# Optimization experiments

Hardware: AMD Instinct MI355X
Metric: run time of the kernel (lower is better)

The kernel has to match this reference:

```python
import jax, jax.numpy as jnp
import numpy as np

N_NODES = 50000
N_EDGES = 800000
N_GRAPHS = 512
IN_DIM, HID, OUT_DIM = 128, 96, 10
N_CONV = 4


def setup_inputs() -> dict:
    key = jax.random.key(0)
    ks = jax.random.split(key, 16)
    s = 0.05
    inp = {
        "x": jax.random.normal(ks[0], (N_NODES, IN_DIM), dtype=jnp.float32),
        "edge_index": jax.random.randint(ks[1], (2, N_EDGES), 0, N_NODES, dtype=jnp.int64),
        "batch": jnp.sort(jax.random.randint(ks[2], (N_NODES,), 0, N_GRAPHS, dtype=jnp.int64)),
        # encoder MLP (2 layers: in->hid, hid->hid)
        "enc_W0": jax.random.normal(ks[3], (IN_DIM, HID), dtype=jnp.float32) * s,
        "enc_b0": jnp.zeros((HID,), dtype=jnp.float32),
        "enc_W1": jax.random.normal(ks[4], (HID, HID), dtype=jnp.float32) * s,
        "enc_b1": jnp.zeros((HID,), dtype=jnp.float32),
        # stacked GCNConv weights
        "conv_W": jax.random.normal(ks[5], (N_CONV, HID, HID), dtype=jnp.float32) * s,
        "conv_b": jnp.zeros((N_CONV, HID), dtype=jnp.float32),
        # decoder MLP (2 layers: hid->hid, hid->out)
        "dec_W0": jax.random.normal(ks[6], (HID, HID), dtype=jnp.float32) * s,
        "dec_b0": jnp.zeros((HID,), dtype=jnp.float32),
        "dec_W1": jax.random.normal(ks[7], (HID, OUT_DIM), dtype=jnp.float32) * s,
        "dec_b1": jnp.zeros((OUT_DIM,), dtype=jnp.float32),
    }
    return inp


def reference(x, edge_index, batch, enc_W0, enc_b0, enc_W1, enc_b1,
              conv_W, conv_b, dec_W0, dec_b0, dec_W1, dec_b1):
    n = x.shape[0]
    src, dst = edge_index[0], edge_index[1]  # source_to_target flow

    # encoder MLP (dropout is identity in eval mode)
    h = jax.nn.relu(x @ enc_W0 + enc_b0)
    h = h @ enc_W1 + enc_b1

    # GCN symmetric normalization with self-loops: deg[i] = in_degree + 1
    deg = jax.ops.segment_sum(jnp.ones_like(dst, dtype=h.dtype), dst, num_segments=n) + 1.0
    dinv = jax.lax.rsqrt(deg)                    # [N]
    edge_norm = (dinv[src] * dinv[dst])[:, None]  # [E,1]
    self_norm = (dinv * dinv)[:, None]            # [N,1] self-loop coefficient

    for l in range(conv_W.shape[0]):
        hw = h @ conv_W[l]                              # linear transform [N,HID]
        msg = hw[src] * edge_norm                       # gather + scale [E,HID]
        h = (jax.ops.segment_sum(msg, dst, num_segments=n)
             + hw * self_norm + conv_b[l])              # scatter-add + self-loop + bias
        h = jax.nn.relu(h)

    # global add pool over graphs in the batch
    g = jax.ops.segment_sum(h, batch, num_segments=N_GRAPHS)  # [G,HID]

    # decoder MLP
    g = jax.nn.relu(g @ dec_W0 + dec_b0)
    return g @ dec_W1 + dec_b1
```

## Files before the change

### kernel.cpp

```cpp
#include <hip/hip_runtime.h>

#define HID 96
#define INDIM 128
#define OUTDIM 10

typedef __attribute__((ext_vector_type(8))) short bf16x8;
typedef __attribute__((ext_vector_type(4))) float f32x4;

__device__ __forceinline__ unsigned short f2bf(float f) {
  unsigned int u = __float_as_uint(f);
  unsigned int r = (u + 0x7FFFu + ((u >> 16) & 1u)) >> 16;
  return (unsigned short)r;
}
__device__ __forceinline__ bf16x8 as_bf16x8(uint4 u) {
  union { uint4 a; bf16x8 b; } c; c.a = u; return c.b;
}
__device__ __forceinline__ float bflo(unsigned int u) { return __uint_as_float(u << 16); }
__device__ __forceinline__ float bfhi(unsigned int u) { return __uint_as_float(u & 0xFFFF0000u); }

__global__ __launch_bounds__(256) void k_prep(const float* __restrict__ x,
                                              unsigned int* __restrict__ xb, long long xu,
                                              int* __restrict__ cnt, int n, int XB,
                                              const float* __restrict__ encW0,
                                              const float* __restrict__ encW1,
                                              const float* __restrict__ convW,
                                              uint4* __restrict__ wp) {
  int b = blockIdx.x;
  if (b < XB) {
    long long i = (long long)b * 256 + threadIdx.x;
    if (i < xu) {
      float2 v = ((const float2*)x)[i];
      xb[i] = (unsigned int)f2bf(v.x) | ((unsigned int)f2bf(v.y) << 16);
    }
    if (i < n) cnt[i] = 0;
    return;
  }
  int bid = b - XB;
  int lane = threadIdx.x;
  if (lane >= 64) return;
  const float* Wsrc;
  int frag;
  if (bid < 24) { Wsrc = encW0; frag = bid; }
  else if (bid < 42) { Wsrc = encW1; frag = bid - 24; }
  else { int c = bid - 42; Wsrc = convW + (size_t)(c / 18) * HID * HID; frag = c % 18; }
  int ks = frag / 6, cf = frag % 6;
  int col = cf * 16 + (lane & 15);
  int k0 = ks * 32 + (lane >> 4) * 8;
  unsigned int u[4];
#pragma unroll
  for (int p = 0; p < 4; ++p) {
    float lo = Wsrc[(size_t)(k0 + 2 * p) * 96 + col];
    float hi = Wsrc[(size_t)(k0 + 2 * p + 1) * 96 + col];
    u[p] = (unsigned int)f2bf(lo) | ((unsigned int)f2bf(hi) << 16);
  }
  uint4 r; r.x = u[0]; r.y = u[1]; r.z = u[2]; r.w = u[3];
  wp[(size_t)bid * 64 + lane] = r;
}

__device__ __forceinline__ void scanA_body(int blk, const int* __restrict__ cnt, int n,
                                           int* __restrict__ bsum, float* __restrict__ dinv) {
  __shared__ int red[256];
  int t = threadIdx.x;
  int base = blk * 512;
  int v = 0;
  int i0 = base + t, i1 = base + 256 + t;
  if (i0 < n) { int c = cnt[i0]; v += c; dinv[i0] = rsqrtf((float)c + 1.0f); }
  if (i1 < n) { int c = cnt[i1]; v += c; dinv[i1] = rsqrtf((float)c + 1.0f); }
  red[t] = v;
  __syncthreads();
  for (int off = 128; off > 0; off >>= 1) {
    if (t < off) red[t] += red[t + off];
    __syncthreads();
  }
  if (t == 0) bsum[blk] = red[0];
}

template <int KS, bool RELU, bool BIAS, bool SCALE>
__device__ __forceinline__ void gemm_body(int blk, const uint4* __restrict__ Ab,
                                          const uint4* __restrict__ Bp,
                                          const float* __restrict__ bias,
                                          const float* __restrict__ rowscale,
                                          unsigned int* __restrict__ outB, int M) {
  int t = threadIdx.x, wid = t >> 6, lane = t & 63;
  int rowbase = blk * 64 + wid * 16;
  int arow = rowbase + (lane & 15);
  if (arow >= M) arow = M - 1;
  constexpr int RU4 = KS * 4;

  f32x4 acc[6];
#pragma unroll
  for (int cf = 0; cf < 6; ++cf)
#pragma unroll
    for (int j = 0; j < 4; ++j) acc[cf][j] = 0.f;

#pragma unroll
  for (int ks = 0; ks < KS; ++ks) {
    uint4 a = Ab[(size_t)arow * RU4 + ks * 4 + (lane >> 4)];
    bf16x8 af = as_bf16x8(a);
#pragma unroll
    for (int cf = 0; cf < 6; ++cf) {
      uint4 b = Bp[(size_t)(ks * 6 + cf) * 64 + lane];
      acc[cf] = __builtin_amdgcn_mfma_f32_16x16x32_bf16(af, as_bf16x8(b), acc[cf], 0, 0, 0);
    }
  }

  int rows[4]; float rs[4];
#pragma unroll
  for (int i = 0; i < 4; ++i) {
    rows[i] = rowbase + (lane >> 4) * 4 + i;
    int cr = rows[i] < M ? rows[i] : M - 1;
    rs[i] = SCALE ? rowscale[cr] : 1.f;
  }
#pragma unroll
  for (int cf = 0; cf < 6; ++cf) {
    int col = cf * 16 + (lane & 15);
    float bv = BIAS ? bias[col] : 0.f;
#pragma unroll
    for (int i = 0; i < 4; ++i) {
      float v = acc[cf][i] + bv;
      if (RELU) v = fmaxf(v, 0.f);
      v *= rs[i];
      float p = __shfl_xor(v, 1);
      if (!(lane & 1) && rows[i] < M) {
        unsigned int u = (unsigned int)f2bf(v) | ((unsigned int)f2bf(p) << 16);
        outB[(size_t)rows[i] * 48 + cf * 8 + ((lane & 15) >> 1)] = u;
      }
    }
  }
}

__global__ __launch_bounds__(256) void k_count_enc1(
    const int4* __restrict__ dst4, int E4, int* __restrict__ cnt, int* __restrict__ rank,
    int CB, const uint4* __restrict__ Ab, const uint4* __restrict__ Bp,
    const float* __restrict__ bias, unsigned int* __restrict__ outB, int M) {
  int b = blockIdx.x;
  if (b < CB) {
    int i = b * 256 + threadIdx.x;
    if (i >= E4) return;
    int4 d = dst4[i];
    int r0 = atomicAdd(&cnt[d.x], 1);
    int r1 = atomicAdd(&cnt[d.y], 1);
    int r2 = atomicAdd(&cnt[d.z], 1);
    int r3 = atomicAdd(&cnt[d.w], 1);
    ((int4*)rank)[i] = make_int4(r0, r1, r2, r3);
  } else {
    gemm_body<4, true, true, false>(b - CB, Ab, Bp, bias, nullptr, outB, M);
  }
}

__global__ __launch_bounds__(256) void k_scanA_enc2(
    const int* __restrict__ cnt, int n, int* __restrict__ bsum, float* __restrict__ dinv,
    int SB, const uint4* __restrict__ Ab, const uint4* __restrict__ Bp,
    const float* __restrict__ bias, unsigned int* __restrict__ outB, int M) {
  int b = blockIdx.x;
  if (b < SB) scanA_body(b, cnt, n, bsum, dinv);
  else gemm_body<3, false, true, false>(b - SB, Ab, Bp, bias, nullptr, outB, M);
}

__global__ __launch_bounds__(256) void k_scanC(const int* __restrict__ cnt, int n,
                                               const int* __restrict__ bsum, int nb,
                                               int* __restrict__ rowp, int Etot) {
  __shared__ int s[256];
  int b = blockIdx.x, t = threadIdx.x;
  int v0 = (t < b && t < nb) ? bsum[t] : 0;
  s[t] = v0;
  __syncthreads();
  for (int off = 128; off > 0; off >>= 1) {
    if (t < off) s[t] += s[t + off];
    __syncthreads();
  }
  int boff = s[0];
  __syncthreads();

  int base = b * 512;
  int i0 = base + 2 * t, i1 = i0 + 1;
  int c0 = (i0 < n) ? cnt[i0] : 0;
  int c1 = (i1 < n) ? cnt[i1] : 0;
  int pair = c0 + c1;
  s[t] = pair;
  __syncthreads();
  for (int off = 1; off < 256; off <<= 1) {
    int u = (t >= off) ? s[t - off] : 0;
    __syncthreads();
    s[t] += u;
    __syncthreads();
  }
  int excl = s[t] - pair + boff;
  if (i0 < n) rowp[i0] = excl;
  if (i1 < n) rowp[i1] = excl + c0;
  if (b == 0 && t == 0) rowp[n] = Etot;
}

__global__ __launch_bounds__(256) void k_fill_conv(
    const int4* __restrict__ src4, const int4* __restrict__ dst4,
    const int4* __restrict__ rank4, int E4, const int* __restrict__ rowp,
    int* __restrict__ csr, int FB, const uint4* __restrict__ Ab,
    const uint4* __restrict__ Bp, const float* __restrict__ rowscale,
    unsigned int* __restrict__ outB, int M) {
  int b = blockIdx.x;
  if (b < FB) {
    int i = b * 256 + threadIdx.x;
    if (i >= E4) return;
    int4 s = src4[i];
    int4 d = dst4[i];
    int4 r = rank4[i];
    csr[rowp[d.x] + r.x] = s.x;
    csr[rowp[d.y] + r.y] = s.y;
    csr[rowp[d.z] + r.z] = s.z;
    csr[rowp[d.w] + r.w] = s.w;
  } else {
    gemm_body<3, false, false, true>(b - FB, Ab, Bp, nullptr, rowscale, outB, M);
  }
}

template <int KS, bool RELU, bool BIAS, bool SCALE>
__global__ __launch_bounds__(256) void mfma_gemm(const uint4* __restrict__ Ab,
                                                 const uint4* __restrict__ Bp,
                                                 const float* __restrict__ bias,
                                                 const float* __restrict__ rowscale,
                                                 unsigned int* __restrict__ outB, int M) {
  gemm_body<KS, RELU, BIAS, SCALE>(blockIdx.x, Ab, Bp, bias, rowscale, outB, M);
}

__global__ __launch_bounds__(256) void k_agg(const unsigned int* __restrict__ hw_s,
                                             const int* __restrict__ rowp,
                                             const int* __restrict__ csr,
                                             const float* __restrict__ dinv,
                                             const float* __restrict__ bias,
                                             unsigned int* __restrict__ outB, int n) {
  int wave = threadIdx.x >> 6;
  int lane = threadIdx.x & 63;
  int node = blockIdx.x * 4 + wave;
  if (node >= n) return;
  int beg = rowp[node], end = rowp[node + 1];
  float acc0 = 0.f, acc1 = 0.f;
  bool act = lane < 48;
  int li = act ? lane : 0;
  int e = beg;
  for (; e + 16 <= end; e += 16) {
    unsigned int uu[16];
#pragma unroll
    for (int j = 0; j < 16; ++j) uu[j] = hw_s[(size_t)csr[e + j] * 48 + li];
    float a0 = 0.f, a1 = 0.f;
#pragma unroll
    for (int j = 0; j < 16; ++j) { a0 += bflo(uu[j]); a1 += bfhi(uu[j]); }
    acc0 += a0; acc1 += a1;
  }
  if (e < end) {
    unsigned int uu[16]; float m[16];
#pragma unroll
    for (int j = 0; j < 16; ++j) {
      int idx = e + j;
      bool ok = idx < end;
      int ci = csr[ok ? idx : end - 1];
      uu[j] = hw_s[(size_t)ci * 48 + li];
      m[j] = ok ? 1.f : 0.f;
    }
    float a0 = 0.f, a1 = 0.f;
#pragma unroll
    for (int j = 0; j < 16; ++j) { a0 += m[j] * bflo(uu[j]); a1 += m[j] * bfhi(uu[j]); }
    acc0 += a0; acc1 += a1;
  }
  if (act) {
    float di = dinv[node];
    unsigned int us = hw_s[(size_t)node * 48 + li];
    float2 bv = ((const float2*)bias)[li];
    float r0 = fmaxf(di * (acc0 + bflo(us)) + bv.x, 0.f);
    float r1 = fmaxf(di * (acc1 + bfhi(us)) + bv.y, 0.f);
    outB[(size_t)node * 48 + li] = (unsigned int)f2bf(r0) | ((unsigned int)f2bf(r1) << 16);
  }
}

__global__ __launch_bounds__(256) void k_head(const unsigned int* __restrict__ hb,
                                              const int* __restrict__ batch, int n,
                                              const float* __restrict__ W0,
                                              const float* __restrict__ b0,
                                              const float* __restrict__ W1,
                                              const float* __restrict__ b1,
                                              float* __restrict__ out) {
  __shared__ float w0L[HID * HID];
  __shared__ float red[4][HID];
  __shared__ float g1L[HID];
  __shared__ float g2L[HID];
  int gr = blockIdx.x;
  int t = threadIdx.x, wv = t >> 6, lane = t & 63;

  for (int i = t; i < HID * HID / 4; i += 256) ((float4*)w0L)[i] = ((const float4*)W0)[i];

  int lo = 0, hi = n;
  while (lo < hi) { int m = (lo + hi) >> 1; if (batch[m] < gr) lo = m + 1; else hi = m; }
  int start = lo;
  hi = n;
  while (lo < hi) { int m = (lo + hi) >> 1; if (batch[m] < gr + 1) lo = m + 1; else hi = m; }
  int end = lo;

  if (lane < 48) {
    float s0 = 0.f, s1 = 0.f;
    for (int i = start + wv; i < end; i += 4) {
      unsigned int u = hb[(size_t)i * 48 + lane];
      s0 += bflo(u);
      s1 += bfhi(u);
    }
    red[wv][2 * lane] = s0;
    red[wv][2 * lane + 1] = s1;
  }
  __syncthreads();
  if (t < HID) g1L[t] = red[0][t] + red[1][t] + red[2][t] + red[3][t];
  __syncthreads();
  if (t < HID) {
    float a = b0[t];
    for (int k = 0; k < HID; ++k) a += g1L[k] * w0L[k * HID + t];
    g2L[t] = fmaxf(a, 0.f);
  }
  __syncthreads();
  if (t < OUTDIM) {
    float a = b1[t];
    for (int k = 0; k < HID; ++k) a += g2L[k] * W1[k * OUTDIM + t];
    out[(size_t)gr * OUTDIM + t] = a;
  }
}

extern "C" void kernel_launch(void* const* d_in, const int* in_sizes, int n_in,
                              void* d_out, int out_size, void* d_ws, size_t ws_size,
                              hipStream_t stream) {
  const float* x     = (const float*)d_in[0];
  const int*   ei    = (const int*)d_in[1];
  const int*   batch = (const int*)d_in[2];
  const float* encW0 = (const float*)d_in[3];
  const float* encb0 = (const float*)d_in[4];
  const float* encW1 = (const float*)d_in[5];
  const float* encb1 = (const float*)d_in[6];
  const float* convW = (const float*)d_in[7];
  const float* convb = (const float*)d_in[8];
  const float* decW0 = (const float*)d_in[9];
  const float* decb0 = (const float*)d_in[10];
  const float* decW1 = (const float*)d_in[11];
  const float* decb1 = (const float*)d_in[12];
  float* out = (float*)d_out;

  int n  = in_sizes[0] / INDIM;
  int E  = in_sizes[1] / 2;
  int G  = out_size / OUTDIM;
  int NC = in_sizes[7] / (HID * HID);

  const int* srcI = ei;
  const int* dstI = ei + E;

  char* w = (char*)d_ws;
  auto alloc = [&](size_t bytes) {
    char* p = w;
    w += (bytes + 255) & ~(size_t)255;
    return p;
  };
  unsigned int* xb  = (unsigned int*)alloc((size_t)n * (INDIM / 2) * 4);
  unsigned int* hbA = (unsigned int*)alloc((size_t)n * 48 * 4);
  unsigned int* hbB = (unsigned int*)alloc((size_t)n * 48 * 4);
  unsigned int* hwb = (unsigned int*)alloc((size_t)n * 48 * 4);
  uint4* wp   = (uint4*)alloc((size_t)(42 + NC * 18) * 64 * 16);
  int*   cnt   = (int*)alloc((size_t)n * 4);
  int*   rankb = (int*)alloc((size_t)E * 4);
  int*   rowp  = (int*)alloc((size_t)(n + 1) * 4);
  int*   csr   = (int*)alloc((size_t)E * 4);
  float* dinv  = (float*)alloc((size_t)n * 4);
  int*   bsum  = (int*)alloc(256 * 4);

  long long xu = (long long)n * (INDIM / 2);
  int XB = (int)((xu + 255) / 256);
  int WB = 42 + NC * 18;
  k_prep<<<XB + WB, 256, 0, stream>>>(x, xb, xu, cnt, n, XB, encW0, encW1, convW, wp);

  int E4 = E / 4;
  int eb4 = (E4 + 255) / 256;
  int nb = (n + 511) / 512;
  int gb = (n + 63) / 64;

  k_count_enc1<<<eb4 + gb, 256, 0, stream>>>((const int4*)dstI, E4, cnt, rankb, eb4,
                                             (const uint4*)xb, wp, encb0, hbA, n);
  k_scanA_enc2<<<nb + gb, 256, 0, stream>>>(cnt, n, bsum, dinv, nb,
                                            (const uint4*)hbA, wp + (size_t)24 * 64,
                                            encb1, hbB, n);
  k_scanC<<<nb, 256, 0, stream>>>(cnt, n, bsum, nb, rowp, E);
  k_fill_conv<<<eb4 + gb, 256, 0, stream>>>((const int4*)srcI, (const int4*)dstI,
                                            (const int4*)rankb, E4, rowp, csr, eb4,
                                            (const uint4*)hbB, wp + (size_t)42 * 64,
                                            dinv, hwb, n);
  k_agg<<<(n + 3) / 4, 256, 0, stream>>>(hwb, rowp, csr, dinv, convb, hbB, n);

  for (int l = 1; l < NC; ++l) {
    mfma_gemm<3, false, false, true><<<gb, 256, 0, stream>>>(
        (const uint4*)hbB, wp + (size_t)(42 + l * 18) * 64, nullptr, dinv, hwb, n);
    k_agg<<<(n + 3) / 4, 256, 0, stream>>>(hwb, rowp, csr, dinv,
                                           convb + (size_t)l * HID, hbB, n);
  }
  k_head<<<G, 256, 0, stream>>>(hbB, batch, n, decW0, decb0, decW1, decb1, out);
}
```

Measured before the change: 248.7 us.

## Fuse GCN aggregation with next layer's linear transform via LDS-staged MFMA

Combines the neighbour aggregation of layer l with the MFMA GEMM of layer l+1 in one kernel. Each 512-thread block aggregates 64 nodes into shared memory as bf16, then runs the 96x96 transform from LDS and writes the dinv-scaled result. This drops a global write and read of the intermediate activations and one launch per layer, and ping-pongs buffers between layers. In exchange, each wave now aggregates 8 nodes one after another, so there are fewer independent nodes in flight to hide gather latency, and the gemm stage waits behind a block-wide barrier.

```diff
diff --git a/kernel.cpp b/kernel.cpp
--- a/kernel.cpp
+++ b/kernel.cpp
@@ -213,13 +213,97 @@
   }
 }
 
-template <int KS, bool RELU, bool BIAS, bool SCALE>
-__global__ __launch_bounds__(256) void mfma_gemm(const uint4* __restrict__ Ab,
-                                                 const uint4* __restrict__ Bp,
-                                                 const float* __restrict__ bias,
-                                                 const float* __restrict__ rowscale,
-                                                 unsigned int* __restrict__ outB, int M) {
-  gemm_body<KS, RELU, BIAS, SCALE>(blockIdx.x, Ab, Bp, bias, rowscale, outB, M);
+__global__ __launch_bounds__(512) void k_agg_gemm(
+    const unsigned int* __restrict__ hw_s, const int* __restrict__ rowp,
+    const int* __restrict__ csr, const float* __restrict__ dinv,
+    const float* __restrict__ bias, const uint4* __restrict__ Bp,
+    unsigned int* __restrict__ outB, int n) {
+  __shared__ unsigned int aL[64 * 52];
+  int t = threadIdx.x, wid = t >> 6, lane = t & 63;
+  int nodebase = blockIdx.x * 64;
+  bool act = lane < 48;
+  int li = act ? lane : 0;
+
+  for (int i = 0; i < 8; ++i) {
+    int lrow = wid * 8 + i;
+    int node = nodebase + lrow;
+    int cn = node < n ? node : n - 1;
+    int beg = rowp[cn], end = rowp[cn + 1];
+    float acc0 = 0.f, acc1 = 0.f;
+    int e = beg;
+    for (; e + 16 <= end; e += 16) {
+      unsigned int uu[16];
+#pragma unroll
+      for (int j = 0; j < 16; ++j) uu[j] = hw_s[(size_t)csr[e + j] * 48 + li];
+      float a0 = 0.f, a1 = 0.f;
+#pragma unroll
+      for (int j = 0; j < 16; ++j) { a0 += bflo(uu[j]); a1 += bfhi(uu[j]); }
+      acc0 += a0; acc1 += a1;
+    }
+    if (e < end) {
+      unsigned int uu[16]; float m[16];
+#pragma unroll
+      for (int j = 0; j < 16; ++j) {
+        int idx = e + j;
+        bool ok = idx < end;
+        int ci = csr[ok ? idx : end - 1];
+        uu[j] = hw_s[(size_t)ci * 48 + li];
+        m[j] = ok ? 1.f : 0.f;
+      }
+      float a0 = 0.f, a1 = 0.f;
+#pragma unroll
+      for (int j = 0; j < 16; ++j) { a0 += m[j] * bflo(uu[j]); a1 += m[j] * bfhi(uu[j]); }
+      acc0 += a0; acc1 += a1;
+    }
+    float di = dinv[cn];
+    unsigned int us = hw_s[(size_t)cn * 48 + li];
+    float2 bv = ((const float2*)bias)[li];
+    float r0 = fmaxf(di * (acc0 + bflo(us)) + bv.x, 0.f);
+    float r1 = fmaxf(di * (acc1 + bfhi(us)) + bv.y, 0.f);
+    if (act) aL[lrow * 52 + li] = (unsigned int)f2bf(r0) | ((unsigned int)f2bf(r1) << 16);
+  }
+  __syncthreads();
+
+  int rb = wid & 3;
+  int cf0 = (wid >> 2) * 3;
+  f32x4 acc[3];
+#pragma unroll
+  for (int j = 0; j < 3; ++j)
+#pragma unroll
+    for (int q = 0; q < 4; ++q) acc[j][q] = 0.f;
+
+  int arow = rb * 16 + (lane & 15);
+#pragma unroll
+  for (int ks = 0; ks < 3; ++ks) {
+    uint4 a = *(const uint4*)&aL[arow * 52 + ks * 16 + (lane >> 4) * 4];
+    bf16x8 af = as_bf16x8(a);
+#pragma unroll
+    for (int j = 0; j < 3; ++j) {
+      uint4 b = Bp[(size_t)(ks * 6 + cf0 + j) * 64 + lane];
+      acc[j] = __builtin_amdgcn_mfma_f32_16x16x32_bf16(af, as_bf16x8(b), acc[j], 0, 0, 0);
+    }
+  }
+
+  int rows[4]; float rs[4];
+#pragma unroll
+  for (int i = 0; i < 4; ++i) {
+    rows[i] = nodebase + rb * 16 + (lane >> 4) * 4 + i;
+    int cr = rows[i] < n ? rows[i] : n - 1;
+    rs[i] = dinv[cr];
+  }
+#pragma unroll
+  for (int j = 0; j < 3; ++j) {
+    int cf = cf0 + j;
+#pragma unroll
+    for (int i = 0; i < 4; ++i) {
+      float v = acc[j][i] * rs[i];
+      float p = __shfl_xor(v, 1);
+      if (!(lane & 1) && rows[i] < n) {
+        unsigned int u = (unsigned int)f2bf(v) | ((unsigned int)f2bf(p) << 16);
+        outB[(size_t)rows[i] * 48 + cf * 8 + ((lane & 15) >> 1)] = u;
+      }
+    }
+  }
 }
 
 __global__ __launch_bounds__(256) void k_agg(const unsigned int* __restrict__ hw_s,
@@ -384,13 +468,15 @@
                                             (const int4*)rankb, E4, rowp, csr, eb4,
                                             (const uint4*)hbB, wp + (size_t)42 * 64,
                                             dinv, hwb, n);
-  k_agg<<<(n + 3) / 4, 256, 0, stream>>>(hwb, rowp, csr, dinv, convb, hbB, n);
-
-  for (int l = 1; l < NC; ++l) {
-    mfma_gemm<3, false, false, true><<<gb, 256, 0, stream>>>(
-        (const uint4*)hbB, wp + (size_t)(42 + l * 18) * 64, nullptr, dinv, hwb, n);
-    k_agg<<<(n + 3) / 4, 256, 0, stream>>>(hwb, rowp, csr, dinv,
-                                           convb + (size_t)l * HID, hbB, n);
-  }
+
+  unsigned int* cur = hwb;
+  unsigned int* nxt = hbA;
+  for (int l = 0; l + 1 < NC; ++l) {
+    k_agg_gemm<<<gb, 512, 0, stream>>>(cur, rowp, csr, dinv, convb + (size_t)l * HID,
+                                       wp + (size_t)(42 + (l + 1) * 18) * 64, nxt, n);
+    unsigned int* tmp = cur; cur = nxt; nxt = tmp;
+  }
+  k_agg<<<(n + 3) / 4, 256, 0, stream>>>(cur, rowp, csr, dinv,
+                                         convb + (size_t)(NC - 1) * HID, hbB, n);
   k_head<<<G, 256, 0, stream>>>(hbB, batch, n, decW0, decb0, decW1, decb1, out);
 }
```

Result: slower. 262.2 us (+5.4%).
